# Optimization experiments

Hardware: AMD Instinct MI355X
Metric: run time of the kernel (lower is better)

## Reference

```python
import jax, jax.numpy as jnp
import numpy as np

B, S_BYTES = 8, 8192
NUM_EMB, BYTE_DIM = 384, 128
EMB_DIM = 1024
NUM_TOKENS = 2048
PAD_ID = 0
SCALE = BYTE_DIM ** 0.5


def setup_inputs() -> dict:
    key = jax.random.key(0)
    k1, k2, k3, k4 = jax.random.split(key, 4)
    x = jax.random.randint(k1, (B, S_BYTES), 0, NUM_EMB, dtype=jnp.int32)
    byte_groups = jnp.sort(
        jax.random.randint(k2, (B, S_BYTES), 0, NUM_TOKENS, dtype=jnp.int32), axis=-1
    )
    # TokenEmbedding init: normal std = byte_dim**-0.5, padding row zeroed
    emb_weight = jax.random.normal(k3, (NUM_EMB, BYTE_DIM), dtype=jnp.float32) * (BYTE_DIM ** -0.5)
    emb_weight = emb_weight.at[PAD_ID].set(0.0)
    # nn.Linear(byte_dim, emb_dim, bias=False): weight [out, in]
    out_proj_w = jax.random.normal(k4, (EMB_DIM, BYTE_DIM), dtype=jnp.float32) * (BYTE_DIM ** -0.5)
    return {"x": x, "byte_groups": byte_groups, "emb_weight": emb_weight, "out_proj_w": out_proj_w}


def _segment_mean(vals, segs):
    # vals: [S, D], segs: [S] sorted segment ids in [0, NUM_TOKENS)
    sums = jax.ops.segment_sum(vals, segs, num_segments=NUM_TOKENS)
    cnts = jax.ops.segment_sum(jnp.ones(segs.shape, vals.dtype), segs, num_segments=NUM_TOKENS)
    return sums / jnp.maximum(cnts, 1.0)[:, None]


def reference(x, byte_groups, emb_weight, out_proj_w):
    # embedding lookup with sqrt(dim) scale: [B, S_bytes, byte_dim]
    byte_emb = emb_weight[x] * jnp.asarray(SCALE, emb_weight.dtype)
    # ragged mean pooling over byte groups -> [B, NUM_TOKENS, byte_dim]
    grouped = jax.vmap(_segment_mean)(byte_emb, byte_groups)
    # out_proj (no bias) -> [B, NUM_TOKENS, emb_dim]; dropout inactive (p=0 / eval)
    emb = jnp.einsum("btd,ed->bte", grouped, out_proj_w)
    return emb
```

## Files before the change

kernel.cpp:

```cpp
#include <hip/hip_runtime.h>
#include <hip/hip_bf16.h>

#define BATCH      8
#define S_BYTES    8192
#define NUM_EMB    384
#define BYTE_DIM   128
#define EMB_DIM    1024
#define NUM_TOKENS 2048
#define SCALE_F    11.313708498984761f

#define M_TOTAL (BATCH * NUM_TOKENS)
#define SEG_STRIDE 2064

typedef __bf16 bf16x8 __attribute__((ext_vector_type(8)));
typedef float  floatx4 __attribute__((ext_vector_type(4)));

__global__ __launch_bounds__(256) void prep_kernel(
    const int* __restrict__ bg,
    int* __restrict__ seg,
    const float* __restrict__ w,
    __hip_bfloat16* __restrict__ wb)
{
    if (blockIdx.x < 256) {
        const int gid = blockIdx.x * 256 + threadIdx.x;
        const int b = gid >> 13;
        const int i = gid & (S_BYTES - 1);
        const int g  = bg[gid];
        const int gp = (i == 0) ? -1 : bg[gid - 1];
        int* __restrict__ srow = seg + b * SEG_STRIDE;
        for (int t = gp + 1; t <= g; ++t) srow[t] = i;
        if (i == S_BYTES - 1) {
            for (int t = g + 1; t <= NUM_TOKENS; ++t) srow[t] = S_BYTES;
        }
    } else {
        const int i = ((blockIdx.x - 256) * 256 + threadIdx.x) * 4;
        const float4 v = *(const float4*)(w + i);
        wb[i + 0] = __float2bfloat16(v.x);
        wb[i + 1] = __float2bfloat16(v.y);
        wb[i + 2] = __float2bfloat16(v.z);
        wb[i + 3] = __float2bfloat16(v.w);
    }
}

__global__ __launch_bounds__(128) void pool_kernel(
    const int* __restrict__ x,
    const int* __restrict__ seg,
    const float* __restrict__ emb,
    __hip_bfloat16* __restrict__ grouped)
{
    const int sub  = threadIdx.x >> 5;
    const int lane = threadIdx.x & 31;
    const int m    = blockIdx.x * 4 + sub;
    const int b    = m >> 11;
    const int t    = m & (NUM_TOKENS - 1);

    const int s   = seg[b * SEG_STRIDE + t];
    const int e   = seg[b * SEG_STRIDE + t + 1];
    const int cnt = e - s;

    const int* __restrict__ xrow = x + b * S_BYTES;
    const float4* __restrict__ embv = (const float4*)emb;

    float4 sum = {0.f, 0.f, 0.f, 0.f};
    #pragma unroll 4
    for (int i = s; i < e; ++i) {
        const int ei = xrow[i];
        const float4 v = embv[ei * 32 + lane];
        sum.x += v.x; sum.y += v.y; sum.z += v.z; sum.w += v.w;
    }
    const float inv = SCALE_F / (float)(cnt > 1 ? cnt : 1);

    __hip_bfloat16 o[4];
    o[0] = __float2bfloat16(sum.x * inv);
    o[1] = __float2bfloat16(sum.y * inv);
    o[2] = __float2bfloat16(sum.z * inv);
    o[3] = __float2bfloat16(sum.w * inv);
    *(uint2*)(grouped + (size_t)m * BYTE_DIM + lane * 4) = *(const uint2*)o;
}

__global__ __launch_bounds__(256) void gemm_kernel(
    const __hip_bfloat16* __restrict__ A,
    const __hip_bfloat16* __restrict__ W,
    float* __restrict__ out)
{
    __shared__ __hip_bfloat16 sA[128 * 128];
    __shared__ __hip_bfloat16 sB[128 * 128];

    const int mb = blockIdx.x & 127;
    const int nb = blockIdx.x >> 7;
    const int m0 = mb * 128;
    const int n0 = nb * 128;
    const int tid = threadIdx.x;

    {
        const bf16x8* __restrict__ gA = (const bf16x8*)(A + (size_t)m0 * BYTE_DIM);
        const bf16x8* __restrict__ gB = (const bf16x8*)(W + (size_t)n0 * BYTE_DIM);
        bf16x8* __restrict__ lA = (bf16x8*)sA;
        bf16x8* __restrict__ lB = (bf16x8*)sB;
        #pragma unroll
        for (int i = 0; i < 8; ++i) {
            lA[tid + i * 256] = gA[tid + i * 256];
            lB[tid + i * 256] = gB[tid + i * 256];
        }
    }
    __syncthreads();

    const int wave = tid >> 6;
    const int lane = tid & 63;
    const int wm = wave >> 1;
    const int wn = wave & 1;
    const int r    = lane & 15;
    const int quad = lane >> 4;

    floatx4 acc[4][4] = {};

    #pragma unroll
    for (int kk = 0; kk < 4; ++kk) {
        bf16x8 af[4], bfr[4];
        #pragma unroll
        for (int i = 0; i < 4; ++i)
            af[i] = *(const bf16x8*)(sA + (wm * 64 + i * 16 + r) * BYTE_DIM + kk * 32 + quad * 8);
        #pragma unroll
        for (int j = 0; j < 4; ++j)
            bfr[j] = *(const bf16x8*)(sB + (wn * 64 + j * 16 + r) * BYTE_DIM + kk * 32 + quad * 8);
        #pragma unroll
        for (int i = 0; i < 4; ++i)
            #pragma unroll
            for (int j = 0; j < 4; ++j)
                acc[i][j] = __builtin_amdgcn_mfma_f32_16x16x32_bf16(af[i], bfr[j], acc[i][j], 0, 0, 0);
    }

    #pragma unroll
    for (int i = 0; i < 4; ++i) {
        const int mrow = m0 + wm * 64 + i * 16 + quad * 4;
        #pragma unroll
        for (int j = 0; j < 4; ++j) {
            const int ncol = n0 + wn * 64 + j * 16 + r;
            float* __restrict__ p = out + (size_t)mrow * EMB_DIM + ncol;
            #pragma unroll
            for (int reg = 0; reg < 4; ++reg)
                p[(size_t)reg * EMB_DIM] = acc[i][j][reg];
        }
    }
}

extern "C" void kernel_launch(void* const* d_in, const int* in_sizes, int n_in,
                              void* d_out, int out_size, void* d_ws, size_t ws_size,
                              hipStream_t stream) {
    const int*   x   = (const int*)d_in[0];
    const int*   bg  = (const int*)d_in[1];
    const float* emb = (const float*)d_in[2];
    const float* w   = (const float*)d_in[3];
    float*       out = (float*)d_out;

    __hip_bfloat16* grouped = (__hip_bfloat16*)d_ws;
    __hip_bfloat16* wb      = (__hip_bfloat16*)((char*)d_ws + (size_t)M_TOTAL * BYTE_DIM * 2);
    int*            seg     = (int*)((char*)d_ws + (size_t)M_TOTAL * BYTE_DIM * 2
                                                 + (size_t)EMB_DIM * BYTE_DIM * 2);

    prep_kernel<<<256 + (EMB_DIM * BYTE_DIM) / (256 * 4), 256, 0, stream>>>(bg, seg, w, wb);
    pool_kernel<<<M_TOTAL / 4, 128, 0, stream>>>(x, seg, emb, grouped);
    gemm_kernel<<<(M_TOTAL / 128) * (EMB_DIM / 128), 256, 0, stream>>>(grouped, wb, out);
}
```

Measured before the change: 96.74 us.

## Fuse segment-mean pooling into GEMM kernel, pooling A tile directly into LDS

Merges the pooling and GEMM kernels so each block pools its 128 tokens straight into shared memory and then computes two 128-column output tiles. This removes the intermediate grouped buffer round-trip through global memory and one kernel launch. In exchange the pooling gather is redone for each of the four column groups, and the grid shrinks to 512 blocks.

```diff
diff --git a/kernel.cpp b/kernel.cpp
--- a/kernel.cpp
+++ b/kernel.cpp
@@ -42,68 +42,56 @@
     }
 }
 
-__global__ __launch_bounds__(128) void pool_kernel(
+__global__ __launch_bounds__(256) void pool_gemm_kernel(
     const int* __restrict__ x,
     const int* __restrict__ seg,
     const float* __restrict__ emb,
-    __hip_bfloat16* __restrict__ grouped)
-{
-    const int sub  = threadIdx.x >> 5;
-    const int lane = threadIdx.x & 31;
-    const int m    = blockIdx.x * 4 + sub;
-    const int b    = m >> 11;
-    const int t    = m & (NUM_TOKENS - 1);
-
-    const int s   = seg[b * SEG_STRIDE + t];
-    const int e   = seg[b * SEG_STRIDE + t + 1];
-    const int cnt = e - s;
-
-    const int* __restrict__ xrow = x + b * S_BYTES;
-    const float4* __restrict__ embv = (const float4*)emb;
-
-    float4 sum = {0.f, 0.f, 0.f, 0.f};
-    #pragma unroll 4
-    for (int i = s; i < e; ++i) {
-        const int ei = xrow[i];
-        const float4 v = embv[ei * 32 + lane];
-        sum.x += v.x; sum.y += v.y; sum.z += v.z; sum.w += v.w;
-    }
-    const float inv = SCALE_F / (float)(cnt > 1 ? cnt : 1);
-
-    __hip_bfloat16 o[4];
-    o[0] = __float2bfloat16(sum.x * inv);
-    o[1] = __float2bfloat16(sum.y * inv);
-    o[2] = __float2bfloat16(sum.z * inv);
-    o[3] = __float2bfloat16(sum.w * inv);
-    *(uint2*)(grouped + (size_t)m * BYTE_DIM + lane * 4) = *(const uint2*)o;
-}
-
-__global__ __launch_bounds__(256) void gemm_kernel(
-    const __hip_bfloat16* __restrict__ A,
-    const __hip_bfloat16* __restrict__ W,
+    const __hip_bfloat16* __restrict__ wb,
     float* __restrict__ out)
 {
     __shared__ __hip_bfloat16 sA[128 * 128];
     __shared__ __hip_bfloat16 sB[128 * 128];
+    __shared__ int sseg[129];
 
-    const int mb = blockIdx.x & 127;
-    const int nb = blockIdx.x >> 7;
-    const int m0 = mb * 128;
-    const int n0 = nb * 128;
-    const int tid = threadIdx.x;
+    const int mb    = blockIdx.x & 127;
+    const int group = blockIdx.x >> 7;
+    const int b     = mb >> 4;
+    const int t0    = (mb & 15) << 7;
+    const int m0    = mb * 128;
+    const int tid   = threadIdx.x;
+
+    if (tid < 129) sseg[tid] = seg[b * SEG_STRIDE + t0 + tid];
+    __syncthreads();
 
     {
-        const bf16x8* __restrict__ gA = (const bf16x8*)(A + (size_t)m0 * BYTE_DIM);
-        const bf16x8* __restrict__ gB = (const bf16x8*)(W + (size_t)n0 * BYTE_DIM);
-        bf16x8* __restrict__ lA = (bf16x8*)sA;
-        bf16x8* __restrict__ lB = (bf16x8*)sB;
-        #pragma unroll
-        for (int i = 0; i < 8; ++i) {
-            lA[tid + i * 256] = gA[tid + i * 256];
-            lB[tid + i * 256] = gB[tid + i * 256];
+        const int sub  = tid >> 5;
+        const int lane = tid & 31;
+        const int* __restrict__ xrow = x + b * S_BYTES;
+        const float4* __restrict__ embv = (const float4*)emb;
+
+        for (int k = 0; k < 16; ++k) {
+            const int tl = sub + k * 8;
+            const int s = sseg[tl];
+            const int e = sseg[tl + 1];
+            const int cnt = e - s;
+
+            float4 sum = {0.f, 0.f, 0.f, 0.f};
+            #pragma unroll 4
+            for (int i = s; i < e; ++i) {
+                const int ei = xrow[i];
+                const float4 v = embv[ei * 32 + lane];
+                sum.x += v.x; sum.y += v.y; sum.z += v.z; sum.w += v.w;
+            }
+            const float inv = SCALE_F / (float)(cnt > 1 ? cnt : 1);
+
+            __hip_bfloat16 o[4];
+            o[0] = __float2bfloat16(sum.x * inv);
+            o[1] = __float2bfloat16(sum.y * inv);
+            o[2] = __float2bfloat16(sum.z * inv);
+            o[3] = __float2bfloat16(sum.w * inv);
+            *(uint2*)(sA + tl * BYTE_DIM + lane * 4) = *(const uint2*)o;
         }
     }
-    __syncthreads();
 
     const int wave = tid >> 6;
     const int lane = tid & 63;
@@ -112,34 +100,46 @@
     const int r    = lane & 15;
     const int quad = lane >> 4;
 
-    floatx4 acc[4][4] = {};
+    for (int q = 0; q < 2; ++q) {
+        const int n0 = (group * 2 + q) * 128;
 
-    #pragma unroll
-    for (int kk = 0; kk < 4; ++kk) {
-        bf16x8 af[4], bfr[4];
+        __syncthreads();
+        {
+            const bf16x8* __restrict__ gB = (const bf16x8*)(wb + (size_t)n0 * BYTE_DIM);
+            bf16x8* __restrict__ lB = (bf16x8*)sB;
+            #pragma unroll
+            for (int i = 0; i < 8; ++i) lB[tid + i * 256] = gB[tid + i * 256];
+        }
+        __syncthreads();
+
+        floatx4 acc[4][4] = {};
         #pragma unroll
-        for (int i = 0; i < 4; ++i)
-            af[i] = *(const bf16x8*)(sA + (wm * 64 + i * 16 + r) * BYTE_DIM + kk * 32 + quad * 8);
-        #pragma unroll
-        for (int j = 0; j < 4; ++j)
-            bfr[j] = *(const bf16x8*)(sB + (wn * 64 + j * 16 + r) * BYTE_DIM + kk * 32 + quad * 8);
-        #pragma unroll
-        for (int i = 0; i < 4; ++i)
+        for (int kk = 0; kk < 4; ++kk) {
+            bf16x8 af[4], bfr[4];
+            #pragma unroll
+            for (int i = 0; i < 4; ++i)
+                af[i] = *(const bf16x8*)(sA + (wm * 64 + i * 16 + r) * BYTE_DIM + kk * 32 + quad * 8);
             #pragma unroll
             for (int j = 0; j < 4; ++j)
-                acc[i][j] = __builtin_amdgcn_mfma_f32_16x16x32_bf16(af[i], bfr[j], acc[i][j], 0, 0, 0);
-    }
+                bfr[j] = *(const bf16x8*)(sB + (wn * 64 + j * 16 + r) * BYTE_DIM + kk * 32 + quad * 8);
+            #pragma unroll
+            for (int i = 0; i < 4; ++i)
+                #pragma unroll
+                for (int j = 0; j < 4; ++j)
+                    acc[i][j] = __builtin_amdgcn_mfma_f32_16x16x32_bf16(af[i], bfr[j], acc[i][j], 0, 0, 0);
+        }
 
-    #pragma unroll
-    for (int i = 0; i < 4; ++i) {
-        const int mrow = m0 + wm * 64 + i * 16 + quad * 4;
         #pragma unroll
-        for (int j = 0; j < 4; ++j) {
-            const int ncol = n0 + wn * 64 + j * 16 + r;
-            float* __restrict__ p = out + (size_t)mrow * EMB_DIM + ncol;
+        for (int i = 0; i < 4; ++i) {
+            const int mrow = m0 + wm * 64 + i * 16 + quad * 4;
             #pragma unroll
-            for (int reg = 0; reg < 4; ++reg)
-                p[(size_t)reg * EMB_DIM] = acc[i][j][reg];
+            for (int j = 0; j < 4; ++j) {
+                const int ncol = n0 + wn * 64 + j * 16 + r;
+                float* __restrict__ p = out + (size_t)mrow * EMB_DIM + ncol;
+                #pragma unroll
+                for (int reg = 0; reg < 4; ++reg)
+                    p[(size_t)reg * EMB_DIM] = acc[i][j][reg];
+            }
         }
     }
 }
@@ -153,12 +153,9 @@
     const float* w   = (const float*)d_in[3];
     float*       out = (float*)d_out;
 
-    __hip_bfloat16* grouped = (__hip_bfloat16*)d_ws;
-    __hip_bfloat16* wb      = (__hip_bfloat16*)((char*)d_ws + (size_t)M_TOTAL * BYTE_DIM * 2);
-    int*            seg     = (int*)((char*)d_ws + (size_t)M_TOTAL * BYTE_DIM * 2
-                                                 + (size_t)EMB_DIM * BYTE_DIM * 2);
+    __hip_bfloat16* wb  = (__hip_bfloat16*)d_ws;
+    int*            seg = (int*)((char*)d_ws + (size_t)EMB_DIM * BYTE_DIM * 2);
 
     prep_kernel<<<256 + (EMB_DIM * BYTE_DIM) / (256 * 4), 256, 0, stream>>>(bg, seg, w, wb);
-    pool_kernel<<<M_TOTAL / 4, 128, 0, stream>>>(x, seg, emb, grouped);
-    gemm_kernel<<<(M_TOTAL / 128) * (EMB_DIM / 128), 256, 0, stream>>>(grouped, wb, out);
+    pool_gemm_kernel<<<512, 256, 0, stream>>>(x, seg, emb, wb, out);
 }
```

Result: slower. 104.3 us (+7.8%).
